# Optimization experiments

Measured on AMD Instinct MI355X. Metric: run time of the kernel, lower is better.

## Reference

```python
import jax, jax.numpy as jnp
import numpy as np

ALPHA = 0.2  # LeakyReLU negative slope
NEG_INF = -9e15


def setup_inputs() -> dict:
    key = jax.random.key(0)
    k1, k2, k3, k4 = jax.random.split(key, 4)
    B, N, Fin, Fout = 8, 2048, 512, 256
    x = jax.random.normal(k1, (B, N, Fin), dtype=jnp.float32)
    adj = jax.random.randint(k2, (B, N, N), 0, 2, dtype=jnp.int32)
    # xavier_uniform-like init, gain=1.414
    limW = 1.414 * np.sqrt(6.0 / (Fin + Fout))
    W = jax.random.uniform(k3, (Fin, Fout), jnp.float32, -limW, limW)
    lima = 1.414 * np.sqrt(6.0 / (2 * Fout + 1))
    a = jax.random.uniform(k4, (2 * Fout, 1), jnp.float32, -lima, lima)
    return {"x": x, "adj": adj, "W": W, "a": a}


def reference(x, adj, W, a):
    # x: [B,N,Fin], adj: [B,N,N], W: [Fin,Fout], a: [2*Fout,1]
    Fout = W.shape[1]
    h = jnp.einsum('bnf,fo->bno', x, W)                      # [B,N,Fout]
    a1 = a[:Fout, 0]                                         # source part
    a2 = a[Fout:, 0]                                         # target part
    # e_ij = LeakyReLU(a1.h_i + a2.h_j) -- decomposed, no O(N^2*2F) tensor
    s = h @ a1                                               # [B,N]
    t = h @ a2                                               # [B,N]
    e = jax.nn.leaky_relu(s[:, :, None] + t[:, None, :], ALPHA)  # [B,N,N]
    e = jnp.where(adj > 0, e, NEG_INF)
    attention = jax.nn.softmax(e, axis=2)                    # dropout p=0 (eval)
    h_prime = jnp.einsum('bij,bjo->bio', attention, h)       # [B,N,Fout]
    return jax.nn.elu(h_prime)                               # concat=True -> ELU
```

## Files before the change

kernel.cpp:

```cpp
#include <hip/hip_runtime.h>
#include <hip/hip_bf16.h>

typedef __attribute__((ext_vector_type(8))) short short8;
typedef __attribute__((ext_vector_type(4))) short short4v;
typedef __attribute__((ext_vector_type(4))) float f32x4;

constexpr int Bb = 8, NN = 2048, FIN = 512, FOUT = 256;
#define LRALPHA 0.2f
#define MFMA16(a, b, c) __builtin_amdgcn_mfma_f32_16x16x32_bf16((a), (b), (c), 0, 0, 0)

static __device__ __forceinline__ ushort f2bf(float f) {
    unsigned u = __float_as_uint(f);
    u += 0x7fffu + ((u >> 16) & 1u);
    return (ushort)(u >> 16);
}
static __device__ __forceinline__ float bf2f(ushort b) { return __uint_as_float(((unsigned)b) << 16); }

#define LDSBAR() do { asm volatile("s_waitcnt lgkmcnt(0)" ::: "memory"); \
                      __builtin_amdgcn_s_barrier(); \
                      asm volatile("" ::: "memory"); } while (0)
#define BARONLY() do { asm volatile("" ::: "memory"); \
                       __builtin_amdgcn_s_barrier(); \
                       asm volatile("" ::: "memory"); } while (0)

__global__ __launch_bounds__(256) void prep(const float* __restrict__ W,
                                            const float* __restrict__ a,
                                            ushort* __restrict__ WTh,
                                            ushort* __restrict__ WTl,
                                            float* __restrict__ wa1,
                                            float* __restrict__ wa2) {
    __shared__ float r1[4], r2[4];
    const int k = blockIdx.x, n = threadIdx.x;
    const int lane = n & 63, wv = n >> 6;
    const float w = W[(size_t)k * FOUT + n];
    const ushort hi = f2bf(w);
    WTh[(size_t)n * FIN + k] = hi;
    WTl[(size_t)n * FIN + k] = f2bf(w - bf2f(hi));
    float p1 = w * a[n], p2 = w * a[FOUT + n];
#pragma unroll
    for (int m = 1; m < 64; m <<= 1) {
        p1 += __shfl_xor(p1, m);
        p2 += __shfl_xor(p2, m);
    }
    if (lane == 0) { r1[wv] = p1; r2[wv] = p2; }
    __syncthreads();
    if (n == 0) {
        wa1[k] = r1[0] + r1[1] + r1[2] + r1[3];
        wa2[k] = r2[0] + r2[1] + r2[2] + r2[3];
    }
}

__global__ __launch_bounds__(512, 4) void gemm_h(const float* __restrict__ x,
                                                 const ushort* __restrict__ WTh,
                                                 const ushort* __restrict__ WTl,
                                                 const float* __restrict__ wa1,
                                                 const float* __restrict__ wa2,
                                                 ushort* __restrict__ hTh,
                                                 float* __restrict__ sv,
                                                 float* __restrict__ tv) {
    __shared__ ushort Ah[4][2][512];
    __shared__ ushort Tr[8][16][72];

    const int t = threadIdx.x, lane = t & 63, w = t >> 6;
    const int m0 = (blockIdx.x >> 1) * 64;
    const int n0 = (blockIdx.x & 1) * 128;

    const int lr = t >> 3, c8 = (t & 7) * 8;
    const int aif = lr >> 4, akstep = c8 >> 5, ak8 = (c8 >> 3) & 3;
    ushort* adst = &Ah[aif][akstep][(((ak8 << 4) | (lr & 15))) * 8];
    const float* xp = x + (size_t)(m0 + lr) * FIN + c8;

    const size_t boff = (size_t)(n0 + w * 16 + (lane & 15)) * FIN + (lane >> 4) * 8;
    const ushort* bph = WTh + boff;
    const ushort* bpl = WTl + boff;

    f32x4 acc[4];
#pragma unroll
    for (int f = 0; f < 4; ++f) acc[f] = (f32x4){0.f, 0.f, 0.f, 0.f};
    float sp = 0.f, tp = 0.f;

    float4 xa0 = *(const float4*)(xp + 0),  xa1 = *(const float4*)(xp + 4);
    float4 xb0 = *(const float4*)(xp + 64), xb1 = *(const float4*)(xp + 68);
    float4 xc0, xc1, xd0, xd1;
    short8 bhA0 = *(const short8*)(bph + 0),  blA0 = *(const short8*)(bpl + 0);
    short8 bhA1 = *(const short8*)(bph + 32), blA1 = *(const short8*)(bpl + 32);
    short8 bhB0, blB0, bhB1, blB1;

    auto phase = [&](int kt, const float4& c0, const float4& c1, float4& nx0, float4& nx1,
                     const short8& cbh0, const short8& cbl0, const short8& cbh1, const short8& cbl1,
                     short8& nbh0, short8& nbl0, short8& nbh1, short8& nbl1) {
        const int k0 = kt * 64;
        const float fv[8] = {c0.x, c0.y, c0.z, c0.w, c1.x, c1.y, c1.z, c1.w};
        short8 vh;
#pragma unroll
        for (int e = 0; e < 8; ++e) vh[e] = (short)f2bf(fv[e]);
        const float4 w1a = *(const float4*)(wa1 + k0 + c8);
        const float4 w1b = *(const float4*)(wa1 + k0 + c8 + 4);
        const float4 w2a = *(const float4*)(wa2 + k0 + c8);
        const float4 w2b = *(const float4*)(wa2 + k0 + c8 + 4);
        sp += fv[0]*w1a.x + fv[1]*w1a.y + fv[2]*w1a.z + fv[3]*w1a.w
            + fv[4]*w1b.x + fv[5]*w1b.y + fv[6]*w1b.z + fv[7]*w1b.w;
        tp += fv[0]*w2a.x + fv[1]*w2a.y + fv[2]*w2a.z + fv[3]*w2a.w
            + fv[4]*w2b.x + fv[5]*w2b.y + fv[6]*w2b.z + fv[7]*w2b.w;
        BARONLY();
        *(short8*)adst = vh;
        LDSBAR();
        const int kx = (kt + 2 < 8 ? kt + 2 : 7) * 64;
        nx0 = *(const float4*)(xp + kx);
        nx1 = *(const float4*)(xp + kx + 4);
        const int kb = (kt + 1 < 8 ? kt + 1 : 7) * 64;
        nbh0 = *(const short8*)(bph + kb);
        nbl0 = *(const short8*)(bpl + kb);
        nbh1 = *(const short8*)(bph + kb + 32);
        nbl1 = *(const short8*)(bpl + kb + 32);
#pragma unroll
        for (int f = 0; f < 4; ++f) {
            const short8 a0 = *(const short8*)&Ah[f][0][lane * 8];
            const short8 a1 = *(const short8*)&Ah[f][1][lane * 8];
            acc[f] = MFMA16(a0, cbh0, acc[f]);
            acc[f] = MFMA16(a0, cbl0, acc[f]);
            acc[f] = MFMA16(a1, cbh1, acc[f]);
            acc[f] = MFMA16(a1, cbl1, acc[f]);
        }
    };

    for (int kt = 0; kt < 8; kt += 4) {
        phase(kt + 0, xa0, xa1, xc0, xc1, bhA0, blA0, bhA1, blA1, bhB0, blB0, bhB1, blB1);
        phase(kt + 1, xb0, xb1, xd0, xd1, bhB0, blB0, bhB1, blB1, bhA0, blA0, bhA1, blA1);
        phase(kt + 2, xc0, xc1, xa0, xa1, bhA0, blA0, bhA1, blA1, bhB0, blB0, bhB1, blB1);
        phase(kt + 3, xd0, xd1, xb0, xb1, bhB0, blB0, bhB1, blB1, bhA0, blA0, bhA1, blA1);
    }

    sp += __shfl_xor(sp, 1, 8); sp += __shfl_xor(sp, 2, 8); sp += __shfl_xor(sp, 4, 8);
    tp += __shfl_xor(tp, 1, 8); tp += __shfl_xor(tp, 2, 8); tp += __shfl_xor(tp, 4, 8);
    if ((t & 7) == 0 && n0 == 0) {
        sv[m0 + lr] = sp;
        tv[m0 + lr] = tp;
    }

    const int rb = (lane >> 4) * 4;
#pragma unroll
    for (int f = 0; f < 4; ++f)
#pragma unroll
        for (int r = 0; r < 4; ++r)
            Tr[w][lane & 15][f * 16 + rb + r] = f2bf(acc[f][r]);
    __syncthreads();
    const int c = lane >> 2, rowb = (lane & 3) * 16;
    const ushort* src = &Tr[w][c][rowb];
    const short8 v0 = *(const short8*)src;
    const short8 v1 = *(const short8*)(src + 8);
    ushort* dst = hTh + ((size_t)(m0 >> 11) * FOUT + n0 + w * 16 + c) * NN + (m0 & 2047) + rowb;
    *(short8*)dst = v0;
    *(short8*)(dst + 8) = v1;
}

__global__ __launch_bounds__(512, 4) void gat_fused(const int* __restrict__ adj,
                                                    const ushort* __restrict__ hTh,
                                                    const float* __restrict__ sv,
                                                    const float* __restrict__ tv,
                                                    float* __restrict__ out) {
    __shared__ float t_l[NN];
    __shared__ ushort Pf[2][2][2][512];
    __shared__ float den_l[32];

    const int t = threadIdx.x, lane = t & 63, w = t >> 6;
    const int b = blockIdx.x & 7, i0 = (blockIdx.x >> 3) * 32;

    *(float4*)&t_l[t * 4] = *(const float4*)&tv[b * NN + t * 4];

    const int r = t >> 4, jn = (t & 15) * 4;
    const float s_i = sv[b * NN + i0 + r];
    const int* adjp = adj + ((size_t)b * NN + i0 + r) * NN + jn;
    const int pif = r >> 4, pkstep = jn >> 5, pk8 = (jn >> 3) & 3;
    const int poff = (((pk8 << 4) | (r & 15))) * 8 + (jn & 4);
    ushort* pdst0 = &Pf[0][pif][pkstep][poff];
    ushort* pdst1 = &Pf[1][pif][pkstep][poff];

    const ushort* hb = hTh + (size_t)b * FOUT * NN;
    const ushort* h00 = hb + (size_t)(2 * w * 16 + (lane & 15)) * NN + (lane >> 4) * 8;
    const ushort* h10 = hb + (size_t)((2 * w + 1) * 16 + (lane & 15)) * NN + (lane >> 4) * 8;

    f32x4 acc00 = {0.f,0.f,0.f,0.f}, acc01 = acc00, acc10 = acc00, acc11 = acc00;
    float den_part = 0.f;

    int4 ajA = *(const int4*)(adjp);
    int4 ajB = *(const int4*)(adjp + 64);
    int4 ajC, ajD;
    short8 X00 = *(const short8*)h00, X01 = *(const short8*)(h00 + 32);
    short8 X10 = *(const short8*)h10, X11 = *(const short8*)(h10 + 32);
    short8 Y00, Y01, Y10, Y11;

    __syncthreads();

    auto phase = [&](int jt, ushort* pdst, int rbuf,
                     const int4& ajcur, int4& aj2,
                     const short8& c00, const short8& c01, const short8& c10, const short8& c11,
                     short8& n00, short8& n01, short8& n10, short8& n11) {
        const int j0 = jt * 64;
        const int jH = min(j0 + 64, NN - 64);
        const int jA = min(j0 + 128, NN - 64);
        n00 = *(const short8*)(h00 + jH);
        n01 = *(const short8*)(h00 + jH + 32);
        n10 = *(const short8*)(h10 + jH);
        n11 = *(const short8*)(h10 + jH + 32);
        aj2 = *(const int4*)(adjp + jA);
        const float4 tq = *(const float4*)&t_l[j0 + jn];
        const float tvv[4] = {tq.x, tq.y, tq.z, tq.w};
        const int avs[4] = {ajcur.x, ajcur.y, ajcur.z, ajcur.w};
        short4v pv;
#pragma unroll
        for (int e = 0; e < 4; ++e) {
            float v = s_i + tvv[e];
            v = v > 0.f ? v : LRALPHA * v;
            const float wv = avs[e] > 0 ? __expf(v) : 0.f;
            const ushort hbv = f2bf(wv);
            den_part += bf2f(hbv);
            pv[e] = (short)hbv;
        }
        *(short4v*)pdst = pv;
        LDSBAR();
        const ushort* pr = &Pf[rbuf][0][0][0] + lane * 8;
        const short8 a00 = *(const short8*)(pr);
        const short8 a01 = *(const short8*)(pr + 512);
        const short8 a10 = *(const short8*)(pr + 1024);
        const short8 a11 = *(const short8*)(pr + 1536);
        __builtin_amdgcn_s_setprio(1);
        acc00 = MFMA16(a00, c00, acc00);
        acc00 = MFMA16(a01, c01, acc00);
        acc01 = MFMA16(a00, c10, acc01);
        acc01 = MFMA16(a01, c11, acc01);
        acc10 = MFMA16(a10, c00, acc10);
        acc10 = MFMA16(a11, c01, acc10);
        acc11 = MFMA16(a10, c10, acc11);
        acc11 = MFMA16(a11, c11, acc11);
        __builtin_amdgcn_s_setprio(0);
    };

    for (int tt = 0; tt < NN / 64; tt += 4) {
        phase(tt + 0, pdst0, 0, ajA, ajC, X00, X01, X10, X11, Y00, Y01, Y10, Y11);
        phase(tt + 1, pdst1, 1, ajB, ajD, Y00, Y01, Y10, Y11, X00, X01, X10, X11);
        phase(tt + 2, pdst0, 0, ajC, ajA, X00, X01, X10, X11, Y00, Y01, Y10, Y11);
        phase(tt + 3, pdst1, 1, ajD, ajB, Y00, Y01, Y10, Y11, X00, X01, X10, X11);
    }

    den_part += __shfl_xor(den_part, 1, 16);
    den_part += __shfl_xor(den_part, 2, 16);
    den_part += __shfl_xor(den_part, 4, 16);
    den_part += __shfl_xor(den_part, 8, 16);
    if ((t & 15) == 0) den_l[r] = den_part;
    __syncthreads();

    const int rb = (lane >> 4) * 4;
    const f32x4 av[2][2] = {{acc00, acc01}, {acc10, acc11}};
#pragma unroll
    for (int f = 0; f < 2; ++f) {
#pragma unroll
        for (int rr = 0; rr < 4; ++rr) {
            const int row = f * 16 + rb + rr;
            const float inv = 1.0f / den_l[row];
#pragma unroll
            for (int cf = 0; cf < 2; ++cf) {
                float v = av[f][cf][rr] * inv;
                v = v > 0.f ? v : expm1f(v);
                out[((size_t)b * NN + i0 + row) * FOUT + w * 32 + cf * 16 + (lane & 15)] = v;
            }
        }
    }
}

extern "C" void kernel_launch(void* const* d_in, const int* in_sizes, int n_in,
                              void* d_out, int out_size, void* d_ws, size_t ws_size,
                              hipStream_t stream) {
    const float* x   = (const float*)d_in[0];
    const int*   adj = (const int*)d_in[1];
    const float* W   = (const float*)d_in[2];
    const float* a   = (const float*)d_in[3];
    float* out = (float*)d_out;

    ushort* hTh = (ushort*)d_ws;
    float*  sv  = (float*)(hTh + (size_t)Bb * FOUT * NN);
    float*  tv  = sv + Bb * NN;
    ushort* WTh = (ushort*)(tv + Bb * NN);
    ushort* WTl = WTh + (size_t)FIN * FOUT;
    float*  wa1 = (float*)(WTl + (size_t)FIN * FOUT);
    float*  wa2 = wa1 + FIN;

    prep<<<FIN, 256, 0, stream>>>(W, a, WTh, WTl, wa1, wa2);
    gemm_h<<<512, 512, 0, stream>>>(x, WTh, WTl, wa1, wa2, hTh, sv, tv);
    gat_fused<<<512, 512, 0, stream>>>(adj, hTh, sv, tv, out);
}
```

Baseline: 303.8 us.

## Double rows per block in fused GAT kernel to halve h reloads

Each block now covers 64 attention rows instead of 32, with each thread computing 8 adjacency weights per tile and four row-fragments of MFMA accumulators. This halves the number of blocks and the global reads of the transposed h matrix per row. In exchange it uses more registers and LDS per block, and the grid is halved (launch bounds lowered to 2), reducing occupancy and latency hiding for the adjacency stream.

```diff
diff --git a/kernel.cpp b/kernel.cpp
--- a/kernel.cpp
+++ b/kernel.cpp
@@ -154,38 +154,42 @@
     *(short8*)(dst + 8) = v1;
 }
 
-__global__ __launch_bounds__(512, 4) void gat_fused(const int* __restrict__ adj,
+__global__ __launch_bounds__(512, 2) void gat_fused(const int* __restrict__ adj,
                                                     const ushort* __restrict__ hTh,
                                                     const float* __restrict__ sv,
                                                     const float* __restrict__ tv,
                                                     float* __restrict__ out) {
     __shared__ float t_l[NN];
-    __shared__ ushort Pf[2][2][2][512];
-    __shared__ float den_l[32];
+    __shared__ ushort Pf[2][4][2][512];
+    __shared__ float den_l[64];
 
     const int t = threadIdx.x, lane = t & 63, w = t >> 6;
-    const int b = blockIdx.x & 7, i0 = (blockIdx.x >> 3) * 32;
+    const int b = blockIdx.x & 7, i0 = (blockIdx.x >> 3) * 64;
 
     *(float4*)&t_l[t * 4] = *(const float4*)&tv[b * NN + t * 4];
 
-    const int r = t >> 4, jn = (t & 15) * 4;
+    const int r = t >> 3, jn = (t & 7) * 8;
     const float s_i = sv[b * NN + i0 + r];
     const int* adjp = adj + ((size_t)b * NN + i0 + r) * NN + jn;
     const int pif = r >> 4, pkstep = jn >> 5, pk8 = (jn >> 3) & 3;
-    const int poff = (((pk8 << 4) | (r & 15))) * 8 + (jn & 4);
-    ushort* pdst0 = &Pf[0][pif][pkstep][poff];
-    ushort* pdst1 = &Pf[1][pif][pkstep][poff];
+    ushort* pdst0 = &Pf[0][pif][pkstep][((pk8 << 4) | (r & 15)) * 8];
+    ushort* pdst1 = &Pf[1][pif][pkstep][((pk8 << 4) | (r & 15)) * 8];
 
     const ushort* hb = hTh + (size_t)b * FOUT * NN;
     const ushort* h00 = hb + (size_t)(2 * w * 16 + (lane & 15)) * NN + (lane >> 4) * 8;
     const ushort* h10 = hb + (size_t)((2 * w + 1) * 16 + (lane & 15)) * NN + (lane >> 4) * 8;
 
-    f32x4 acc00 = {0.f,0.f,0.f,0.f}, acc01 = acc00, acc10 = acc00, acc11 = acc00;
+    f32x4 acc[4][2];
+#pragma unroll
+    for (int f = 0; f < 4; ++f) {
+        acc[f][0] = (f32x4){0.f, 0.f, 0.f, 0.f};
+        acc[f][1] = (f32x4){0.f, 0.f, 0.f, 0.f};
+    }
     float den_part = 0.f;
 
-    int4 ajA = *(const int4*)(adjp);
-    int4 ajB = *(const int4*)(adjp + 64);
-    int4 ajC, ajD;
+    int4 ajA0 = *(const int4*)(adjp),      ajA1 = *(const int4*)(adjp + 4);
+    int4 ajB0 = *(const int4*)(adjp + 64), ajB1 = *(const int4*)(adjp + 68);
+    int4 ajC0, ajC1, ajD0, ajD1;
     short8 X00 = *(const short8*)h00, X01 = *(const short8*)(h00 + 32);
     short8 X10 = *(const short8*)h10, X11 = *(const short8*)(h10 + 32);
     short8 Y00, Y01, Y10, Y11;
@@ -193,7 +197,7 @@
     __syncthreads();
 
     auto phase = [&](int jt, ushort* pdst, int rbuf,
-                     const int4& ajcur, int4& aj2,
+                     const int4& ac0, const int4& ac1, int4& an0, int4& an1,
                      const short8& c00, const short8& c01, const short8& c10, const short8& c11,
                      short8& n00, short8& n01, short8& n10, short8& n11) {
         const int j0 = jt * 64;
@@ -203,13 +207,15 @@
         n01 = *(const short8*)(h00 + jH + 32);
         n10 = *(const short8*)(h10 + jH);
         n11 = *(const short8*)(h10 + jH + 32);
-        aj2 = *(const int4*)(adjp + jA);
-        const float4 tq = *(const float4*)&t_l[j0 + jn];
-        const float tvv[4] = {tq.x, tq.y, tq.z, tq.w};
-        const int avs[4] = {ajcur.x, ajcur.y, ajcur.z, ajcur.w};
-        short4v pv;
-#pragma unroll
-        for (int e = 0; e < 4; ++e) {
+        an0 = *(const int4*)(adjp + jA);
+        an1 = *(const int4*)(adjp + jA + 4);
+        const float4 tq0 = *(const float4*)&t_l[j0 + jn];
+        const float4 tq1 = *(const float4*)&t_l[j0 + jn + 4];
+        const float tvv[8] = {tq0.x, tq0.y, tq0.z, tq0.w, tq1.x, tq1.y, tq1.z, tq1.w};
+        const int avs[8] = {ac0.x, ac0.y, ac0.z, ac0.w, ac1.x, ac1.y, ac1.z, ac1.w};
+        short8 pv;
+#pragma unroll
+        for (int e = 0; e < 8; ++e) {
             float v = s_i + tvv[e];
             v = v > 0.f ? v : LRALPHA * v;
             const float wv = avs[e] > 0 ? __expf(v) : 0.f;
@@ -217,50 +223,45 @@
             den_part += bf2f(hbv);
             pv[e] = (short)hbv;
         }
-        *(short4v*)pdst = pv;
+        *(short8*)pdst = pv;
         LDSBAR();
         const ushort* pr = &Pf[rbuf][0][0][0] + lane * 8;
-        const short8 a00 = *(const short8*)(pr);
-        const short8 a01 = *(const short8*)(pr + 512);
-        const short8 a10 = *(const short8*)(pr + 1024);
-        const short8 a11 = *(const short8*)(pr + 1536);
         __builtin_amdgcn_s_setprio(1);
-        acc00 = MFMA16(a00, c00, acc00);
-        acc00 = MFMA16(a01, c01, acc00);
-        acc01 = MFMA16(a00, c10, acc01);
-        acc01 = MFMA16(a01, c11, acc01);
-        acc10 = MFMA16(a10, c00, acc10);
-        acc10 = MFMA16(a11, c01, acc10);
-        acc11 = MFMA16(a10, c10, acc11);
-        acc11 = MFMA16(a11, c11, acc11);
+#pragma unroll
+        for (int f = 0; f < 4; ++f) {
+            const short8 a0 = *(const short8*)(pr + f * 1024);
+            const short8 a1 = *(const short8*)(pr + f * 1024 + 512);
+            acc[f][0] = MFMA16(a0, c00, acc[f][0]);
+            acc[f][0] = MFMA16(a1, c01, acc[f][0]);
+            acc[f][1] = MFMA16(a0, c10, acc[f][1]);
+            acc[f][1] = MFMA16(a1, c11, acc[f][1]);
+        }
         __builtin_amdgcn_s_setprio(0);
     };
 
     for (int tt = 0; tt < NN / 64; tt += 4) {
-        phase(tt + 0, pdst0, 0, ajA, ajC, X00, X01, X10, X11, Y00, Y01, Y10, Y11);
-        phase(tt + 1, pdst1, 1, ajB, ajD, Y00, Y01, Y10, Y11, X00, X01, X10, X11);
-        phase(tt + 2, pdst0, 0, ajC, ajA, X00, X01, X10, X11, Y00, Y01, Y10, Y11);
-        phase(tt + 3, pdst1, 1, ajD, ajB, Y00, Y01, Y10, Y11, X00, X01, X10, X11);
-    }
-
-    den_part += __shfl_xor(den_part, 1, 16);
-    den_part += __shfl_xor(den_part, 2, 16);
-    den_part += __shfl_xor(den_part, 4, 16);
-    den_part += __shfl_xor(den_part, 8, 16);
-    if ((t & 15) == 0) den_l[r] = den_part;
+        phase(tt + 0, pdst0, 0, ajA0, ajA1, ajC0, ajC1, X00, X01, X10, X11, Y00, Y01, Y10, Y11);
+        phase(tt + 1, pdst1, 1, ajB0, ajB1, ajD0, ajD1, Y00, Y01, Y10, Y11, X00, X01, X10, X11);
+        phase(tt + 2, pdst0, 0, ajC0, ajC1, ajA0, ajA1, X00, X01, X10, X11, Y00, Y01, Y10, Y11);
+        phase(tt + 3, pdst1, 1, ajD0, ajD1, ajB0, ajB1, Y00, Y01, Y10, Y11, X00, X01, X10, X11);
+    }
+
+    den_part += __shfl_xor(den_part, 1, 8);
+    den_part += __shfl_xor(den_part, 2, 8);
+    den_part += __shfl_xor(den_part, 4, 8);
+    if ((t & 7) == 0) den_l[r] = den_part;
     __syncthreads();
 
     const int rb = (lane >> 4) * 4;
-    const f32x4 av[2][2] = {{acc00, acc01}, {acc10, acc11}};
-#pragma unroll
-    for (int f = 0; f < 2; ++f) {
+#pragma unroll
+    for (int f = 0; f < 4; ++f) {
 #pragma unroll
         for (int rr = 0; rr < 4; ++rr) {
             const int row = f * 16 + rb + rr;
             const float inv = 1.0f / den_l[row];
 #pragma unroll
             for (int cf = 0; cf < 2; ++cf) {
-                float v = av[f][cf][rr] * inv;
+                float v = acc[f][cf][rr] * inv;
                 v = v > 0.f ? v : expm1f(v);
                 out[((size_t)b * NN + i0 + row) * FOUT + w * 32 + cf * 16 + (lane & 15)] = v;
             }
@@ -287,5 +288,5 @@
 
     prep<<<FIN, 256, 0, stream>>>(W, a, WTh, WTl, wa1, wa2);
     gemm_h<<<512, 512, 0, stream>>>(x, WTh, WTl, wa1, wa2, hTh, sv, tv);
-    gat_fused<<<512, 512, 0, stream>>>(adj, hTh, sv, tv, out);
-}
+    gat_fused<<<256, 512, 0, stream>>>(adj, hTh, sv, tv, out);
+}
```

Result: faster. 270.5 us (-11.0%).
